# Kernel optimization log

Hardware: AMD Instinct MI355X
Metric: run time of the kernel (lower is better)

The kernel has to match this reference:

```python
import jax, jax.numpy as jnp
import numpy as np

N, E, G = 65536, 262144, 2048
DIN, H, F, L, P, TASK = 9, 300, 32, 5, 3, 1
DG = H + F + 1024 + 167  # 1523


def setup_inputs() -> dict:
    key = jax.random.key(0)
    ks = jax.random.split(key, 24)
    s = 0.02
    inp = {
        'x': jax.random.normal(ks[0], (N, DIN), jnp.float32),
        'morgan': jax.random.uniform(ks[1], (G, 1024), jnp.float32),
        'maccs': jax.random.uniform(ks[2], (G, 167), jnp.float32),
        'edge_index': jax.random.randint(ks[3], (2, E), 0, N, jnp.int32),
        'batch': jnp.sort(jax.random.randint(ks[4], (N,), 0, G, jnp.int32)),
        # node feature encoder
        'W_emb': s * jax.random.normal(ks[5], (DIN, H), jnp.float32),
        'b_emb': jnp.zeros((H,), jnp.float32),
        # GIN conv MLPs (L layers): H -> 2H -> H
        'gin_W1': s * jax.random.normal(ks[6], (L, H, 2 * H), jnp.float32),
        'gin_b1': jnp.zeros((L, 2 * H), jnp.float32),
        'gin_W2': s * jax.random.normal(ks[7], (L, 2 * H, H), jnp.float32),
        'gin_b2': jnp.zeros((L, H), jnp.float32),
        'bn_scale': jnp.ones((L, H), jnp.float32),
        'bn_bias': jnp.zeros((L, H), jnp.float32),
        'eps': jnp.zeros((L,), jnp.float32),
        # virtual node: init embedding + update MLPs (L-1 layers)
        'vn0': jnp.zeros((H,), jnp.float32),
        'vn_W1': s * jax.random.normal(ks[8], (L - 1, H, 2 * H), jnp.float32),
        'vn_b1': jnp.zeros((L - 1, 2 * H), jnp.float32),
        'vn_W2': s * jax.random.normal(ks[9], (L - 1, 2 * H, H), jnp.float32),
        'vn_b2': jnp.zeros((L - 1, H), jnp.float32),
        # predictor MLP: DG -> 2H -> TASK
        'Wp1': s * jax.random.normal(ks[10], (DG, 2 * H), jnp.float32),
        'bp1': jnp.zeros((2 * H,), jnp.float32),
        'Wp2': s * jax.random.normal(ks[11], (2 * H, TASK), jnp.float32),
        'bp2': jnp.zeros((TASK,), jnp.float32),
    }
    return inp


def _seg_mean(v, seg, n):
    s = jax.ops.segment_sum(v, seg, num_segments=n)
    c = jax.ops.segment_sum(jnp.ones((v.shape[0], 1), v.dtype), seg, num_segments=n)
    return s / jnp.maximum(c, 1.0)


def _bn(z, scale, bias):
    m = z.mean(0)
    v = z.var(0)
    return (z - m) * jax.lax.rsqrt(v + 1e-5) * scale + bias


def _gnn_and_predict(x, morgan, maccs, W_emb, b_emb, gin_W1, gin_b1, gin_W2, gin_b2,
                     bn_scale, bn_bias, eps, vn0, vn_W1, vn_b1, vn_W2, vn_b2,
                     Wp1, bp1, Wp2, bp2, edge_index, batch):
    n = x.shape[0]
    g = morgan.shape[0]
    nl = gin_W1.shape[0]
    src, dst = edge_index[0], edge_index[1]

    # GIN-virtual backbone (eval mode, dropout off). Note: GNN input is the
    # original x (the permuted ids are appended AFTER the GNN), so h is
    # permutation-independent and computed once.
    h = x @ W_emb + b_emb
    vn = jnp.broadcast_to(vn0, (g, vn0.shape[0]))
    for l in range(nl):
        hv = h + vn[batch]                                       # [N,H]
        agg = jax.ops.segment_sum(hv[src], dst, num_segments=n)  # neighbor sum
        z = (1.0 + eps[l]) * hv + agg
        z = jax.nn.relu(z @ gin_W1[l] + gin_b1[l]) @ gin_W2[l] + gin_b2[l]
        z = _bn(z, bn_scale[l], bn_bias[l])
        if l < nl - 1:
            z = jax.nn.relu(z)
        h = h + z  # residual
        if l < nl - 1:  # virtual node update
            vt = jax.ops.segment_sum(hv, batch, num_segments=g) + vn
            vn = vn + jax.nn.relu(jax.nn.relu(vt @ vn_W1[l] + vn_b1[l]) @ vn_W2[l] + vn_b2[l])

    pooled_h = _seg_mean(h, batch, g)  # [G,H]

    # Segmented random permutation of tiled eye(F) ids, averaged over P perms.
    # Each node gets one_hot(perm_rank_within_graph % F); rank computed by a
    # single lexsort over (batch, random) instead of a per-graph Python loop.
    counts = jax.ops.segment_sum(jnp.ones((n,), jnp.int32), batch, num_segments=g)
    starts = jnp.concatenate([jnp.zeros((1,), jnp.int32),
                              jnp.cumsum(counts)[:-1].astype(jnp.int32)])
    pkey = jax.random.key(42)
    acc = jnp.zeros((g, F), h.dtype)
    for p in range(P):
        r = jax.random.uniform(jax.random.fold_in(pkey, p), (n,))
        order = jnp.lexsort((r, batch))                       # sort by graph, then random
        local = jnp.arange(n, dtype=jnp.int32) - starts[batch[order]]
        rank = jnp.zeros((n,), jnp.int32).at[order].set(local)  # random rank in graph
        ids = jax.nn.one_hot(rank % F, F, dtype=h.dtype)        # [N,F]
        acc = acc + _seg_mean(ids, batch, g)
    id_pool = acc / P

    # h_rep order matches torch: [pooled h | pooled ids | morgan | maccs]
    h_rep = jnp.concatenate([pooled_h, id_pool, morgan, maccs], axis=1)  # [G,1523]
    return jax.nn.relu(h_rep @ Wp1 + bp1) @ Wp2 + bp2  # [G,TASK]


def reference(x, morgan, maccs, W_emb, b_emb, gin_W1, gin_b1, gin_W2, gin_b2,
              bn_scale, bn_bias, eps, vn0, vn_W1, vn_b1, vn_W2, vn_b2,
              Wp1, bp1, Wp2, bp2, edge_index, batch):
    return _gnn_and_predict(x, morgan, maccs, W_emb, b_emb, gin_W1, gin_b1,
                            gin_W2, gin_b2, bn_scale, bn_bias, eps, vn0,
                            vn_W1, vn_b1, vn_W2, vn_b2, Wp1, bp1, Wp2, bp2,
                            edge_index, batch)
```

## Files before the change

kernel.cpp:

```cpp
#include <hip/hip_runtime.h>

typedef unsigned short u16;
typedef unsigned int u32;
typedef __attribute__((ext_vector_type(8))) short bf16x8_t;
typedef __attribute__((ext_vector_type(4))) float f32x4_t;

#define kN 65536
#define kE 262144
#define kG 2048
#define kH 300
#define kH2 600
#define kL 5
#define kF 32
#define kDG 1523
#define KP_H 320
#define KP_H2 640
#define KP_DG 1536
#define NP_H2 640
#define NP_H 320
#define HVS 320
#define HVS32 160

__device__ __forceinline__ float bf2f(u16 x) {
    union { u32 u; float f; } v; v.u = ((u32)x) << 16; return v.f;
}
__device__ __forceinline__ u16 f2bf(float f) {
    union { float f; u32 u; } v; v.f = f;
    u32 u = v.u;
    u32 r = (u + 0x7fffu + ((u >> 16) & 1u)) >> 16;
    return (u16)r;
}
__device__ __forceinline__ float blo(u32 v) { return bf2f((u16)(v & 0xffffu)); }
__device__ __forceinline__ float bhi(u32 v) { return bf2f((u16)(v >> 16)); }
__device__ __forceinline__ u32 pack2(float lo, float hi) {
    return (u32)f2bf(lo) | ((u32)f2bf(hi) << 16);
}

__device__ __forceinline__ void gld16(const u16* g, u16* l) {
    __builtin_amdgcn_global_load_lds(
        (const __attribute__((address_space(1))) u32*)g,
        (__attribute__((address_space(3))) u32*)l, 16, 0, 0);
}

__device__ __forceinline__ void vwait4() { asm volatile("s_waitcnt vmcnt(4)" ::: "memory"); }
__device__ __forceinline__ void vwait6() { asm volatile("s_waitcnt vmcnt(6)" ::: "memory"); }
__device__ __forceinline__ void vwait8() { asm volatile("s_waitcnt vmcnt(8)" ::: "memory"); }
__device__ __forceinline__ void vwait0() { asm volatile("s_waitcnt vmcnt(0)" ::: "memory"); }
__device__ __forceinline__ void rbar() {
    __builtin_amdgcn_sched_barrier(0);
    __builtin_amdgcn_s_barrier();
    __builtin_amdgcn_sched_barrier(0);
}

__device__ __forceinline__ void swz_tile(int& m, int& n) {
    int p = blockIdx.x + gridDim.x * blockIdx.y;
    int xcd = p & 7;
    int q = p >> 3;
    int NB = gridDim.y;
    int mb8 = gridDim.x >> 3;
    m = xcd * mb8 + q / NB;
    n = q % NB;
}

__global__ void transpose_k(const float* __restrict__ W, u16* __restrict__ Wt,
                            int K, int NN, int NP, int KP, long total) {
    long idx = (long)blockIdx.x * 256 + threadIdx.x;
    if (idx >= total) return;
    int per = NP * KP;
    int b = (int)(idx / per);
    int r = (int)(idx % per);
    int n = r / KP;
    int k = r % KP;
    u16 v = 0;
    if (n < NN && k < K) v = f2bf(W[(long)b * K * NN + (long)k * NN + n]);
    Wt[idx] = v;
}

__global__ void hist_g_k(const int* __restrict__ batch, int* __restrict__ counts) {
    int n = blockIdx.x * 256 + threadIdx.x;
    if (n < kN) atomicAdd(&counts[batch[n]], 1);
}

__global__ void scan_g_k(const int* __restrict__ counts, int* __restrict__ starts) {
    __shared__ int s[1024];
    int t = threadIdx.x;
    int c0 = counts[2 * t], c1 = counts[2 * t + 1];
    s[t] = c0 + c1;
    __syncthreads();
    for (int off = 1; off < 1024; off <<= 1) {
        int v = (t >= off) ? s[t - off] : 0;
        __syncthreads();
        s[t] += v;
        __syncthreads();
    }
    int excl = (t > 0) ? s[t - 1] : 0;
    starts[2 * t] = excl;
    starts[2 * t + 1] = excl + c0;
}

__global__ void hist_n_k(const int* __restrict__ ei, int* __restrict__ cnt) {
    int e = blockIdx.x * 256 + threadIdx.x;
    if (e < kE) atomicAdd(&cnt[ei[kE + e]], 1);
}

__global__ void scanA_k(const int* __restrict__ cnt, int* __restrict__ start, int* __restrict__ bsum) {
    __shared__ int s[1024];
    int b = blockIdx.x, t = threadIdx.x;
    int v = cnt[b * 1024 + t];
    s[t] = v;
    __syncthreads();
    for (int off = 1; off < 1024; off <<= 1) {
        int u = (t >= off) ? s[t - off] : 0;
        __syncthreads();
        s[t] += u;
        __syncthreads();
    }
    start[b * 1024 + t] = s[t] - v;
    if (t == 1023) bsum[b] = s[1023];
}

__global__ void scanB_k(int* __restrict__ bsum) {
    if (threadIdx.x == 0) {
        int s = 0;
        for (int i = 0; i < kN / 1024; i++) { s += bsum[i]; bsum[i] = s; }
    }
}

__global__ void scanC_k(int* __restrict__ start, const int* __restrict__ bsum) {
    int b = blockIdx.x, t = threadIdx.x;
    int add = (b > 0) ? bsum[b - 1] : 0;
    start[b * 1024 + t] += add;
    if (b == kN / 1024 - 1 && t == 1023) start[kN] = bsum[kN / 1024 - 1];
}

__global__ void fill_n_k(const int* __restrict__ ei, const int* __restrict__ start,
                         int* __restrict__ fill, int* __restrict__ perm) {
    int e = blockIdx.x * 256 + threadIdx.x;
    if (e >= kE) return;
    int s = ei[e], d = ei[kE + e];
    int pos = start[d] + atomicAdd(&fill[d], 1);
    perm[pos] = s;
}

__global__ __launch_bounds__(256) void embed_k(
    const float* __restrict__ x, const float* __restrict__ W,
    const float* __restrict__ b, const float* __restrict__ vn0,
    u32* __restrict__ hv32) {
    __shared__ float sW[9 * kH];
    __shared__ float sBV[kH];
    int tid = threadIdx.x;
    for (int i = tid; i < 9 * kH; i += 256) sW[i] = W[i];
    for (int i = tid; i < kH; i += 256) sBV[i] = b[i] + vn0[i];
    __syncthreads();
    int wave = tid >> 6, lane = tid & 63;
    int n = blockIdx.x * 4 + wave;
    float xv[9];
    #pragma unroll
    for (int d = 0; d < 9; d++) xv[d] = x[n * 9 + d];
    #pragma unroll
    for (int p = 0; p < 3; p++) {
        int ii = lane + p * 64;
        if (ii < 150) {
            int c0 = 2 * ii;
            float a0 = sBV[c0], a1 = sBV[c0 + 1];
            #pragma unroll
            for (int d = 0; d < 9; d++) {
                a0 += xv[d] * sW[d * kH + c0];
                a1 += xv[d] * sW[d * kH + c0 + 1];
            }
            hv32[(long)n * HVS32 + ii] = pack2(a0, a1);
        } else if (ii < HVS32) {
            hv32[(long)n * HVS32 + ii] = 0u;
        }
    }
}

__global__ void vninit_k(const float* __restrict__ vn0, float* __restrict__ vn) {
    int g = blockIdx.x, c = threadIdx.x;
    if (c < kH) vn[g * kH + c] = vn0[c];
}

__global__ __launch_bounds__(256) void gather_combine_k(
    const u32* __restrict__ hv32, const int* __restrict__ start_n,
    const int* __restrict__ perm, const float* __restrict__ eps, int l,
    u32* __restrict__ out32, float* __restrict__ stats) {
    int tid = threadIdx.x;
    int wave = tid >> 6, lane = tid & 63;
    int n = blockIdx.x * 4 + wave;
    int st = start_n[n], en = start_n[n + 1];
    int i0 = lane, i1 = lane + 64, i2 = lane + 128;
    bool p2 = (i2 < 150);
    float a0 = 0.f, b0 = 0.f, a1 = 0.f, b1 = 0.f, a2 = 0.f, b2 = 0.f;
    int e = st;
    for (; e + 4 <= en; e += 4) {
        const u32* rA = hv32 + (long)perm[e] * HVS32;
        const u32* rB = hv32 + (long)perm[e + 1] * HVS32;
        const u32* rC = hv32 + (long)perm[e + 2] * HVS32;
        const u32* rD = hv32 + (long)perm[e + 3] * HVS32;
        u32 vA0 = rA[i0], vA1 = rA[i1], vA2 = p2 ? rA[i2] : 0u;
        u32 vB0 = rB[i0], vB1 = rB[i1], vB2 = p2 ? rB[i2] : 0u;
        u32 vC0 = rC[i0], vC1 = rC[i1], vC2 = p2 ? rC[i2] : 0u;
        u32 vD0 = rD[i0], vD1 = rD[i1], vD2 = p2 ? rD[i2] : 0u;
        a0 += (blo(vA0) + blo(vB0)) + (blo(vC0) + blo(vD0));
        b0 += (bhi(vA0) + bhi(vB0)) + (bhi(vC0) + bhi(vD0));
        a1 += (blo(vA1) + blo(vB1)) + (blo(vC1) + blo(vD1));
        b1 += (bhi(vA1) + bhi(vB1)) + (bhi(vC1) + bhi(vD1));
        a2 += (blo(vA2) + blo(vB2)) + (blo(vC2) + blo(vD2));
        b2 += (bhi(vA2) + bhi(vB2)) + (bhi(vC2) + bhi(vD2));
    }
    for (; e + 2 <= en; e += 2) {
        const u32* rA = hv32 + (long)perm[e] * HVS32;
        const u32* rB = hv32 + (long)perm[e + 1] * HVS32;
        u32 vA0 = rA[i0], vA1 = rA[i1], vA2 = p2 ? rA[i2] : 0u;
        u32 vB0 = rB[i0], vB1 = rB[i1], vB2 = p2 ? rB[i2] : 0u;
        a0 += blo(vA0) + blo(vB0); b0 += bhi(vA0) + bhi(vB0);
        a1 += blo(vA1) + blo(vB1); b1 += bhi(vA1) + bhi(vB1);
        a2 += blo(vA2) + blo(vB2); b2 += bhi(vA2) + bhi(vB2);
    }
    if (e < en) {
        const u32* rA = hv32 + (long)perm[e] * HVS32;
        u32 vA0 = rA[i0], vA1 = rA[i1], vA2 = p2 ? rA[i2] : 0u;
        a0 += blo(vA0); b0 += bhi(vA0);
        a1 += blo(vA1); b1 += bhi(vA1);
        a2 += blo(vA2); b2 += bhi(vA2);
    }
    const u32* self = hv32 + (long)n * HVS32;
    float ep = 1.f + eps[l];
    u32 s0 = self[i0], s1 = self[i1];
    u32* o = out32 + (long)n * HVS32;
    o[i0] = pack2(ep * blo(s0) + a0, ep * bhi(s0) + b0);
    o[i1] = pack2(ep * blo(s1) + a1, ep * bhi(s1) + b1);
    if (p2) {
        u32 s2 = self[i2];
        o[i2] = pack2(ep * blo(s2) + a2, ep * bhi(s2) + b2);
    } else if (i2 < HVS32) {
        o[i2] = 0u;
    }
    int gz = blockIdx.x * 256 + tid;
    if (gz < 2 * kH) stats[gz] = 0.f;
}

__global__ __launch_bounds__(256) void vt_fin_k(
    const u32* __restrict__ hv32, const float* __restrict__ vncur,
    const int* __restrict__ counts, const int* __restrict__ starts,
    u32* __restrict__ vt32) {
    int tid = threadIdx.x, wave = tid >> 6, lane = tid & 63;
    int g = blockIdx.x * 4 + wave;
    int cnt = counts[g], st = starts[g];
    int i0 = lane, i1 = lane + 64, i2 = lane + 128;
    bool p2 = (i2 < 150);
    float a0 = 0.f, b0 = 0.f, a1 = 0.f, b1 = 0.f, a2 = 0.f, b2 = 0.f;
    int i = 0;
    for (; i + 4 <= cnt; i += 4) {
        const u32* rA = hv32 + (long)(st + i) * HVS32;
        const u32* rB = hv32 + (long)(st + i + 1) * HVS32;
        const u32* rC = hv32 + (long)(st + i + 2) * HVS32;
        const u32* rD = hv32 + (long)(st + i + 3) * HVS32;
        u32 vA0 = rA[i0], vA1 = rA[i1], vA2 = p2 ? rA[i2] : 0u;
        u32 vB0 = rB[i0], vB1 = rB[i1], vB2 = p2 ? rB[i2] : 0u;
        u32 vC0 = rC[i0], vC1 = rC[i1], vC2 = p2 ? rC[i2] : 0u;
        u32 vD0 = rD[i0], vD1 = rD[i1], vD2 = p2 ? rD[i2] : 0u;
        a0 += (blo(vA0) + blo(vB0)) + (blo(vC0) + blo(vD0));
        b0 += (bhi(vA0) + bhi(vB0)) + (bhi(vC0) + bhi(vD0));
        a1 += (blo(vA1) + blo(vB1)) + (blo(vC1) + blo(vD1));
        b1 += (bhi(vA1) + bhi(vB1)) + (bhi(vC1) + bhi(vD1));
        a2 += (blo(vA2) + blo(vB2)) + (blo(vC2) + blo(vD2));
        b2 += (bhi(vA2) + bhi(vB2)) + (bhi(vC2) + bhi(vD2));
    }
    for (; i < cnt; i++) {
        const u32* rA = hv32 + (long)(st + i) * HVS32;
        u32 vA0 = rA[i0], vA1 = rA[i1], vA2 = p2 ? rA[i2] : 0u;
        a0 += blo(vA0); b0 += bhi(vA0);
        a1 += blo(vA1); b1 += bhi(vA1);
        a2 += blo(vA2); b2 += bhi(vA2);
    }
    const float* vg = vncur + g * kH;
    vt32[(long)g * HVS32 + i0] = pack2(a0 + vg[2 * i0], b0 + vg[2 * i0 + 1]);
    vt32[(long)g * HVS32 + i1] = pack2(a1 + vg[2 * i1], b1 + vg[2 * i1 + 1]);
    if (p2) vt32[(long)g * HVS32 + i2] = pack2(a2 + vg[2 * i2], b2 + vg[2 * i2 + 1]);
    else if (i2 < HVS32) vt32[(long)g * HVS32 + i2] = 0u;
}

__global__ __launch_bounds__(512, 2) void fused_mlp_k(
    const u16* __restrict__ A,
    const u16* __restrict__ W1t,
    const float* __restrict__ b1,
    const u16* __restrict__ W2t,
    const float* __restrict__ b2,
    u16* __restrict__ outp,
    float* __restrict__ stats) {
    __shared__ __align__(16) u16 lA[2][128 * 64];
    __shared__ __align__(16) u16 lW1[2][128 * 64];
    __shared__ __align__(16) u16 z1c[128 * 128];
    __shared__ __align__(16) u16 lW2[320 * 64];
    __shared__ float sred[320][2];

    const int tid = threadIdx.x;
    const int lane = tid & 63;
    const int wave = tid >> 6;
    const int l16 = lane & 15;
    const int quad = lane >> 4;
    const long tm = (long)blockIdx.x * 128;
    const int srow = lane >> 3;
    const int sch = (lane & 7) ^ srow;

    const int wm = (wave & 1) * 64;
    const int wnA = (wave >> 1) * 32;
    const int wnB = (wave >> 1) * 80;

    if (tid < 320) { sred[tid][0] = 0.f; sred[tid][1] = 0.f; }

    float rb1[5][2];
    #pragma unroll
    for (int c = 0; c < 5; c++)
        #pragma unroll
        for (int nt = 0; nt < 2; nt++) {
            int gc = c * 128 + wnA + nt * 16 + l16;
            rb1[c][nt] = (gc < kH2) ? b1[gc] : 0.f;
        }
    float rb2[5];
    #pragma unroll
    for (int nt = 0; nt < 5; nt++) {
        int col = wnB + nt * 16 + l16;
        rb2[nt] = (col < kH) ? b2[col] : 0.f;
    }

    f32x4_t acc2[4][5];
    #pragma unroll
    for (int i = 0; i < 4; i++)
        #pragma unroll
        for (int j = 0; j < 5; j++) acc2[i][j] = (f32x4_t){0.f, 0.f, 0.f, 0.f};

    for (int c = 0; c < 5; c++) {
        f32x4_t acc1[4][2];
        #pragma unroll
        for (int i = 0; i < 4; i++) {
            acc1[i][0] = (f32x4_t){0.f, 0.f, 0.f, 0.f};
            acc1[i][1] = (f32x4_t){0.f, 0.f, 0.f, 0.f};
        }
        auto stageA = [&](int bb, int k0) {
            #pragma unroll
            for (int j = 0; j < 2; j++) {
                int rb = wave * 16 + j * 8;
                gld16(A + (tm + rb + srow) * KP_H + k0 + sch * 8, &lA[bb][rb * 64]);
                gld16(W1t + (long)(c * 128 + rb + srow) * KP_H + k0 + sch * 8, &lW1[bb][rb * 64]);
            }
        };
        stageA(0, 0);
        stageA(1, 64);
        for (int t = 0; t < 5; t++) {
            if (t < 4) vwait4(); else vwait0();
            rbar();
            const u16* la = lA[t & 1];
            const u16* lw = lW1[t & 1];
            #pragma unroll
            for (int ks = 0; ks < 2; ks++) {
                bf16x8_t af[4], bfr[2];
                #pragma unroll
                for (int mt = 0; mt < 4; mt++) {
                    int row = wm + mt * 16 + l16;
                    int phys = (ks * 4 + quad) ^ (l16 & 7);
                    af[mt] = *(const bf16x8_t*)&la[row * 64 + phys * 8];
                }
                #pragma unroll
                for (int nt = 0; nt < 2; nt++) {
                    int row = wnA + nt * 16 + l16;
                    int phys = (ks * 4 + quad) ^ (l16 & 7);
                    bfr[nt] = *(const bf16x8_t*)&lw[row * 64 + phys * 8];
                }
                #pragma unroll
                for (int mt = 0; mt < 4; mt++)
                    #pragma unroll
                    for (int nt = 0; nt < 2; nt++)
                        acc1[mt][nt] = __builtin_amdgcn_mfma_f32_16x16x32_bf16(af[mt], bfr[nt], acc1[mt][nt], 0, 0, 0);
            }
            rbar();
            if (t + 2 < 5) stageA(t & 1, (t + 2) * 64);
        }

        #pragma unroll
        for (int j = 0; j < 5; j++) {
            int rb = wave * 40 + j * 8;
            gld16(W2t + (long)(rb + srow) * KP_H2 + c * 128 + sch * 8, &lW2[rb * 64]);
        }

        #pragma unroll
        for (int nt = 0; nt < 2; nt++) {
            int col = wnA + nt * 16 + l16;
            #pragma unroll
            for (int mt = 0; mt < 4; mt++) {
                #pragma unroll
                for (int r = 0; r < 4; r++) {
                    int row = wm + mt * 16 + quad * 4 + r;
                    float v = acc1[mt][nt][r] + rb1[c][nt];
                    v = fmaxf(v, 0.f);
                    int phys = (col >> 3) ^ (row & 15);
                    z1c[row * 128 + phys * 8 + (col & 7)] = f2bf(v);
                }
            }
        }
        __syncthreads();

        #pragma unroll
        for (int s = 0; s < 2; s++) {
            #pragma unroll
            for (int ks = 0; ks < 2; ks++) {
                bf16x8_t af[4], bfr[5];
                #pragma unroll
                for (int mt = 0; mt < 4; mt++) {
                    int row = wm + mt * 16 + l16;
                    int phys = (s * 8 + ks * 4 + quad) ^ (row & 15);
                    af[mt] = *(const bf16x8_t*)&z1c[row * 128 + phys * 8];
                }
                #pragma unroll
                for (int nt = 0; nt < 5; nt++) {
                    int row = wnB + nt * 16 + l16;
                    int phys = (ks * 4 + quad) ^ (l16 & 7);
                    bfr[nt] = *(const bf16x8_t*)&lW2[row * 64 + phys * 8];
                }
                #pragma unroll
                for (int mt = 0; mt < 4; mt++)
                    #pragma unroll
                    for (int nt = 0; nt < 5; nt++)
                        acc2[mt][nt] = __builtin_amdgcn_mfma_f32_16x16x32_bf16(af[mt], bfr[nt], acc2[mt][nt], 0, 0, 0);
            }
            rbar();
            if (s == 0) {
                #pragma unroll
                for (int j = 0; j < 5; j++) {
                    int rb = wave * 40 + j * 8;
                    gld16(W2t + (long)(rb + srow) * KP_H2 + c * 128 + 64 + sch * 8, &lW2[rb * 64]);
                }
                vwait0();
                rbar();
            }
        }
    }

    #pragma unroll
    for (int nt = 0; nt < 5; nt++) {
        int col = wnB + nt * 16 + l16;
        float s = 0.f, s2 = 0.f;
        #pragma unroll
        for (int mt = 0; mt < 4; mt++) {
            #pragma unroll
            for (int r = 0; r < 4; r++) {
                long row = tm + wm + mt * 16 + quad * 4 + r;
                float v = acc2[mt][nt][r] + rb2[nt];
                float sv = (col < kH) ? v : 0.f;
                outp[row * KP_H + col] = f2bf(sv);
                s += sv; s2 += sv * sv;
            }
        }
        atomicAdd(&sred[col][0], s);
        atomicAdd(&sred[col][1], s2);
    }
    __syncthreads();
    if (tid < kH) {
        atomicAdd(&stats[tid], sred[tid][0]);
        atomicAdd(&stats[kH + tid], sred[tid][1]);
    }
}

template<int ACT, int OUT_BF16, int BN_STATS>
__global__ __launch_bounds__(256) void gemm_k(
    const u16* __restrict__ A, const u16* __restrict__ Wt,
    const float* __restrict__ bias, void* __restrict__ out,
    float* __restrict__ stats,
    int KP, int NN, int out_stride, int store_cols) {
    __shared__ __align__(16) u16 lA[2][128 * 64];
    __shared__ __align__(16) u16 lB[2][128 * 64];
    __shared__ float sred[128][2];

    const int tid = threadIdx.x;
    const int lane = tid & 63;
    const int wave = tid >> 6;
    const int l16 = lane & 15;
    const int quad = lane >> 4;
    const int wm = (wave & 1) * 64;
    const int wn = (wave >> 1) * 64;
    int sm, sn;
    swz_tile(sm, sn);
    const long tm = (long)sm * 128;
    const int tn = sn * 128;

    const int srow = lane >> 3;
    const int sch = (lane & 7) ^ srow;

    f32x4_t acc[4][4];
    #pragma unroll
    for (int i = 0; i < 4; i++)
        #pragma unroll
        for (int j = 0; j < 4; j++) acc[i][j] = (f32x4_t){0.f, 0.f, 0.f, 0.f};

    auto stage = [&](int bb, int k0) {
        #pragma unroll
        for (int j = 0; j < 4; j++) {
            int rb = wave * 32 + j * 8;
            int r = rb + srow;
            gld16(A + (tm + r) * KP + k0 + sch * 8, &lA[bb][rb * 64]);
            gld16(Wt + (long)(tn + r) * KP + k0 + sch * 8, &lB[bb][rb * 64]);
        }
    };

    const int nk = KP >> 6;
    stage(0, 0);
    if (nk > 1) stage(1, 64);
    for (int t = 0; t < nk; t++) {
        if (t < nk - 1) vwait8(); else vwait0();
        rbar();
        const u16* la = lA[t & 1];
        const u16* lb = lB[t & 1];
        #pragma unroll
        for (int ks = 0; ks < 2; ks++) {
            bf16x8_t af[4], bfr[4];
            #pragma unroll
            for (int mt = 0; mt < 4; mt++) {
                int row = wm + mt * 16 + l16;
                int phys = (ks * 4 + quad) ^ (l16 & 7);
                af[mt] = *(const bf16x8_t*)&la[row * 64 + phys * 8];
            }
            #pragma unroll
            for (int nt = 0; nt < 4; nt++) {
                int row = wn + nt * 16 + l16;
                int phys = (ks * 4 + quad) ^ (l16 & 7);
                bfr[nt] = *(const bf16x8_t*)&lb[row * 64 + phys * 8];
            }
            #pragma unroll
            for (int mt = 0; mt < 4; mt++)
                #pragma unroll
                for (int nt = 0; nt < 4; nt++)
                    acc[mt][nt] = __builtin_amdgcn_mfma_f32_16x16x32_bf16(af[mt], bfr[nt], acc[mt][nt], 0, 0, 0);
        }
        rbar();
        if (t + 2 < nk) stage(t & 1, (t + 2) * 64);
    }

    if (BN_STATS) {
        if (tid < 128) { sred[tid][0] = 0.f; sred[tid][1] = 0.f; }
    }
    __syncthreads();

    #pragma unroll
    for (int nt = 0; nt < 4; nt++) {
        int col = tn + wn + nt * 16 + l16;
        float bv = (col < NN) ? bias[col] : 0.f;
        float s = 0.f, s2 = 0.f;
        #pragma unroll
        for (int mt = 0; mt < 4; mt++) {
            #pragma unroll
            for (int r = 0; r < 4; r++) {
                long row = tm + wm + mt * 16 + quad * 4 + r;
                float v = acc[mt][nt][r] + bv;
                if (ACT) v = fmaxf(v, 0.f);
                float sv = (col < NN) ? v : 0.f;
                if (col < store_cols) {
                    if (OUT_BF16) ((u16*)out)[row * out_stride + col] = f2bf(sv);
                    else          ((float*)out)[row * out_stride + col] = sv;
                }
                s += sv; s2 += sv * sv;
            }
        }
        if (BN_STATS) {
            atomicAdd(&sred[wn + nt * 16 + l16][0], s);
            atomicAdd(&sred[wn + nt * 16 + l16][1], s2);
        }
    }
    if (BN_STATS) {
        __syncthreads();
        if (tid < 128) {
            int col = tn + tid;
            if (col < NN) {
                atomicAdd(&stats[col], sred[tid][0]);
                atomicAdd(&stats[NN + col], sred[tid][1]);
            }
        }
    }
}

template<int ACT, int OUT_MODE, int BN_STATS>
__global__ __launch_bounds__(256) void gemm64_k(
    const u16* __restrict__ A, const u16* __restrict__ Wt,
    const float* __restrict__ bias, void* __restrict__ out,
    float* __restrict__ stats, const float* __restrict__ vnacc,
    int KP, int NN, int out_stride, int store_cols) {
    __shared__ __align__(16) u16 lA[2][128 * 64];
    __shared__ __align__(16) u16 lB[2][64 * 64];
    __shared__ float sred[64][2];

    const int tid = threadIdx.x;
    const int lane = tid & 63;
    const int wave = tid >> 6;
    const int l16 = lane & 15;
    const int quad = lane >> 4;
    const int wm = (wave & 1) * 64;
    const int wn = (wave >> 1) * 32;
    int sm, sn;
    swz_tile(sm, sn);
    const long tm = (long)sm * 128;
    const int tn = sn * 64;

    const int srow = lane >> 3;
    const int sch = (lane & 7) ^ srow;

    f32x4_t acc[4][2];
    #pragma unroll
    for (int i = 0; i < 4; i++)
        #pragma unroll
        for (int j = 0; j < 2; j++) acc[i][j] = (f32x4_t){0.f, 0.f, 0.f, 0.f};

    auto stage = [&](int bb, int k0) {
        #pragma unroll
        for (int j = 0; j < 4; j++) {
            int rb = wave * 32 + j * 8;
            gld16(A + (tm + rb + srow) * KP + k0 + sch * 8, &lA[bb][rb * 64]);
        }
        #pragma unroll
        for (int j = 0; j < 2; j++) {
            int rb = wave * 16 + j * 8;
            gld16(Wt + (long)(tn + rb + srow) * KP + k0 + sch * 8, &lB[bb][rb * 64]);
        }
    };

    const int nk = KP >> 6;
    stage(0, 0);
    if (nk > 1) stage(1, 64);
    for (int t = 0; t < nk; t++) {
        if (t < nk - 1) vwait6(); else vwait0();
        rbar();
        const u16* la = lA[t & 1];
        const u16* lb = lB[t & 1];
        #pragma unroll
        for (int ks = 0; ks < 2; ks++) {
            bf16x8_t af[4], bfr[2];
            #pragma unroll
            for (int mt = 0; mt < 4; mt++) {
                int row = wm + mt * 16 + l16;
                int phys = (ks * 4 + quad) ^ (l16 & 7);
                af[mt] = *(const bf16x8_t*)&la[row * 64 + phys * 8];
            }
            #pragma unroll
            for (int nt = 0; nt < 2; nt++) {
                int row = wn + nt * 16 + l16;
                int phys = (ks * 4 + quad) ^ (l16 & 7);
                bfr[nt] = *(const bf16x8_t*)&lb[row * 64 + phys * 8];
            }
            #pragma unroll
            for (int mt = 0; mt < 4; mt++)
                #pragma unroll
                for (int nt = 0; nt < 2; nt++)
                    acc[mt][nt] = __builtin_amdgcn_mfma_f32_16x16x32_bf16(af[mt], bfr[nt], acc[mt][nt], 0, 0, 0);
        }
        rbar();
        if (t + 2 < nk) stage(t & 1, (t + 2) * 64);
    }

    if (BN_STATS) {
        if (tid < 64) { sred[tid][0] = 0.f; sred[tid][1] = 0.f; }
    }
    __syncthreads();

    #pragma unroll
    for (int nt = 0; nt < 2; nt++) {
        int col = tn + wn + nt * 16 + l16;
        float bv = (col < NN) ? bias[col] : 0.f;
        float s = 0.f, s2 = 0.f;
        #pragma unroll
        for (int mt = 0; mt < 4; mt++) {
            #pragma unroll
            for (int r = 0; r < 4; r++) {
                long row = tm + wm + mt * 16 + quad * 4 + r;
                float v = acc[mt][nt][r] + bv;
                if (ACT) v = fmaxf(v, 0.f);
                float sv = (col < NN) ? v : 0.f;
                if (col < store_cols) {
                    if (OUT_MODE == 1) ((u16*)out)[row * out_stride + col] = f2bf(sv);
                    else if (OUT_MODE == 2)
                        ((float*)out)[row * out_stride + col] =
                            vnacc[row * out_stride + col] + fmaxf(v, 0.f);
                    else ((float*)out)[row * out_stride + col] = sv;
                }
                s += sv; s2 += sv * sv;
            }
        }
        if (BN_STATS) {
            atomicAdd(&sred[wn + nt * 16 + l16][0], s);
            atomicAdd(&sred[wn + nt * 16 + l16][1], s2);
        }
    }
    if (BN_STATS) {
        __syncthreads();
        if (tid < 64) {
            int col = tn + tid;
            if (col < NN) {
                atomicAdd(&stats[col], sred[tid][0]);
                atomicAdd(&stats[NN + col], sred[tid][1]);
            }
        }
    }
}

template<int RELU>
__global__ __launch_bounds__(256) void resid_k(
    u32* __restrict__ hvb32, const u32* __restrict__ z32,
    const float* __restrict__ stats,
    const float* __restrict__ scale, const float* __restrict__ bias, int l,
    const int* __restrict__ batch,
    const float* __restrict__ vncur, const float* __restrict__ vnnxt) {
    int tid = threadIdx.x;
    int wave = tid >> 6, lane = tid & 63;
    int n = blockIdx.x * 4 + wave;
    int g = batch[n];
    #pragma unroll
    for (int p = 0; p < 3; p++) {
        int ii = lane + p * 64;
        if (ii >= 150) break;
        int c0 = 2 * ii;
        float m0 = stats[c0] * (1.f / (float)kN), m1 = stats[c0 + 1] * (1.f / (float)kN);
        float v0 = fmaxf(stats[kH + c0] * (1.f / (float)kN) - m0 * m0, 0.f);
        float v1 = fmaxf(stats[kH + c0 + 1] * (1.f / (float)kN) - m1 * m1, 0.f);
        float a0 = scale[l * kH + c0] * rsqrtf(v0 + 1e-5f);
        float a1 = scale[l * kH + c0 + 1] * rsqrtf(v1 + 1e-5f);
        float d0 = bias[l * kH + c0] - m0 * a0;
        float d1 = bias[l * kH + c0 + 1] - m1 * a1;
        u32 zz = z32[(long)n * HVS32 + ii];
        u32 ho = hvb32[(long)n * HVS32 + ii];
        float2 vc = *(const float2*)(vncur + g * kH + c0);
        float2 vx = *(const float2*)(vnnxt + g * kH + c0);
        float t0 = blo(zz) * a0 + d0;
        float t1 = bhi(zz) * a1 + d1;
        if (RELU) { t0 = fmaxf(t0, 0.f); t1 = fmaxf(t1, 0.f); }
        float h0 = (blo(ho) - vc.x) + t0;
        float h1 = (bhi(ho) - vc.y) + t1;
        hvb32[(long)n * HVS32 + ii] = pack2(h0 + vx.x, h1 + vx.y);
    }
}

__global__ __launch_bounds__(256) void pooled_k(
    const u32* __restrict__ hv32, const float* __restrict__ vnlast,
    const int* __restrict__ counts, const int* __restrict__ starts,
    u32* __restrict__ hrep32) {
    int tid = threadIdx.x, wave = tid >> 6, lane = tid & 63;
    int g = blockIdx.x * 4 + wave;
    int cnt = counts[g], st = starts[g];
    int i0 = lane, i1 = lane + 64, i2 = lane + 128;
    bool p2 = (i2 < 150);
    float a0 = 0.f, b0 = 0.f, a1 = 0.f, b1 = 0.f, a2 = 0.f, b2 = 0.f;
    int i = 0;
    for (; i + 4 <= cnt; i += 4) {
        const u32* rA = hv32 + (long)(st + i) * HVS32;
        const u32* rB = hv32 + (long)(st + i + 1) * HVS32;
        const u32* rC = hv32 + (long)(st + i + 2) * HVS32;
        const u32* rD = hv32 + (long)(st + i + 3) * HVS32;
        u32 vA0 = rA[i0], vA1 = rA[i1], vA2 = p2 ? rA[i2] : 0u;
        u32 vB0 = rB[i0], vB1 = rB[i1], vB2 = p2 ? rB[i2] : 0u;
        u32 vC0 = rC[i0], vC1 = rC[i1], vC2 = p2 ? rC[i2] : 0u;
        u32 vD0 = rD[i0], vD1 = rD[i1], vD2 = p2 ? rD[i2] : 0u;
        a0 += (blo(vA0) + blo(vB0)) + (blo(vC0) + blo(vD0));
        b0 += (bhi(vA0) + bhi(vB0)) + (bhi(vC0) + bhi(vD0));
        a1 += (blo(vA1) + blo(vB1)) + (blo(vC1) + blo(vD1));
        b1 += (bhi(vA1) + bhi(vB1)) + (bhi(vC1) + bhi(vD1));
        a2 += (blo(vA2) + blo(vB2)) + (blo(vC2) + blo(vD2));
        b2 += (bhi(vA2) + bhi(vB2)) + (bhi(vC2) + bhi(vD2));
    }
    for (; i < cnt; i++) {
        const u32* rA = hv32 + (long)(st + i) * HVS32;
        u32 vA0 = rA[i0], vA1 = rA[i1], vA2 = p2 ? rA[i2] : 0u;
        a0 += blo(vA0); b0 += bhi(vA0);
        a1 += blo(vA1); b1 += bhi(vA1);
        a2 += blo(vA2); b2 += bhi(vA2);
    }
    float fc = (float)cnt;
    float inv = 1.f / (float)(cnt > 0 ? cnt : 1);
    const float* vg = vnlast + g * kH;
    hrep32[(long)g * 768 + i0] = pack2((a0 - fc * vg[2 * i0]) * inv, (b0 - fc * vg[2 * i0 + 1]) * inv);
    hrep32[(long)g * 768 + i1] = pack2((a1 - fc * vg[2 * i1]) * inv, (b1 - fc * vg[2 * i1 + 1]) * inv);
    if (p2)
        hrep32[(long)g * 768 + i2] = pack2((a2 - fc * vg[2 * i2]) * inv, (b2 - fc * vg[2 * i2 + 1]) * inv);
}

__global__ void hrep_rest_k(const float* __restrict__ morgan, const float* __restrict__ maccs,
                            const int* __restrict__ counts, u16* __restrict__ hrep) {
    long idx = (long)blockIdx.x * 256 + threadIdx.x;
    if (idx >= (long)kG * (KP_DG - kH)) return;
    int g = (int)(idx / (KP_DG - kH));
    int j = (int)(idx % (KP_DG - kH));
    int col = kH + j;
    u16 v;
    if (j < kF) {
        int c = counts[g];
        int q = (j < c) ? ((c - 1 - j) / kF + 1) : 0;
        v = f2bf((float)q / (float)(c > 0 ? c : 1));
    } else if (j < kF + 1024) {
        v = f2bf(morgan[(long)g * 1024 + (j - kF)]);
    } else if (j < kF + 1024 + 167) {
        v = f2bf(maccs[(long)g * 167 + (j - kF - 1024)]);
    } else {
        v = 0;
    }
    hrep[(long)g * KP_DG + col] = v;
}

__global__ void final_k(const u16* __restrict__ zp, const float* __restrict__ Wp2,
                        const float* __restrict__ bp2, float* __restrict__ out) {
    int wave = threadIdx.x >> 6, lane = threadIdx.x & 63;
    int g = blockIdx.x * 4 + wave;
    float acc = 0.f;
    for (int c = lane; c < kH2; c += 64) acc += bf2f(zp[(long)g * KP_H2 + c]) * Wp2[c];
    #pragma unroll
    for (int off = 32; off; off >>= 1) acc += __shfl_down(acc, off);
    if (lane == 0) out[g] = acc + bp2[0];
}

extern "C" void kernel_launch(void* const* d_in, const int* in_sizes, int n_in,
                              void* d_out, int out_size, void* d_ws, size_t ws_size,
                              hipStream_t stream) {
    const float* x      = (const float*)d_in[0];
    const float* morgan = (const float*)d_in[1];
    const float* maccs  = (const float*)d_in[2];
    const int*   ei     = (const int*)d_in[3];
    const int*   batch  = (const int*)d_in[4];
    const float* W_emb  = (const float*)d_in[5];
    const float* b_emb  = (const float*)d_in[6];
    const float* gin_W1 = (const float*)d_in[7];
    const float* gin_b1 = (const float*)d_in[8];
    const float* gin_W2 = (const float*)d_in[9];
    const float* gin_b2 = (const float*)d_in[10];
    const float* bn_scale = (const float*)d_in[11];
    const float* bn_bias  = (const float*)d_in[12];
    const float* eps    = (const float*)d_in[13];
    const float* vn0    = (const float*)d_in[14];
    const float* vn_W1  = (const float*)d_in[15];
    const float* vn_b1  = (const float*)d_in[16];
    const float* vn_W2  = (const float*)d_in[17];
    const float* vn_b2  = (const float*)d_in[18];
    const float* Wp1    = (const float*)d_in[19];
    const float* bp1    = (const float*)d_in[20];
    const float* Wp2    = (const float*)d_in[21];
    const float* bp2    = (const float*)d_in[22];
    float* out = (float*)d_out;

    char* ws = (char*)d_ws;
    size_t off = 0;
    auto alloc = [&](size_t bytes) -> char* {
        char* p = ws + off;
        off += (bytes + 255) & ~(size_t)255;
        return p;
    };
    u16*   hvbf = (u16*)alloc((size_t)kN * HVS * 2);
    u16*   hv   = (u16*)alloc((size_t)kN * KP_H * 2);
    u16*   z1   = (u16*)alloc((size_t)kN * KP_H2 * 2);
    float* vnA  = (float*)alloc((size_t)kG * kH * 4);
    float* vnB  = (float*)alloc((size_t)kG * kH * 4);
    int* counts = (int*)alloc(kG * 4);
    int* starts = (int*)alloc(kG * 4);
    float* stats = (float*)alloc(2 * kH * 4);
    int* cnt_n  = (int*)alloc((size_t)kN * 4);
    int* start_n = (int*)alloc((size_t)(kN + 1) * 4);
    int* fill_n = (int*)alloc((size_t)kN * 4);
    int* bsum   = (int*)alloc((kN / 1024) * 4);
    int* perm   = (int*)alloc((size_t)kE * 4);
    u16* Wt_g1 = (u16*)alloc((size_t)kL * NP_H2 * KP_H * 2);
    u16* Wt_g2 = (u16*)alloc((size_t)kL * NP_H * KP_H2 * 2);
    u16* Wt_v1 = (u16*)alloc((size_t)(kL - 1) * NP_H2 * KP_H * 2);
    u16* Wt_v2 = (u16*)alloc((size_t)(kL - 1) * NP_H * KP_H2 * 2);
    u16* Wt_p1 = (u16*)alloc((size_t)NP_H2 * KP_DG * 2);
    if (off > ws_size) return;

    u16* vt_in = z1;
    u16* z1v   = z1 + (size_t)4 * 1024 * 1024;
    u16* hrep  = z1;
    u16* zp    = z1 + (size_t)8 * 1024 * 1024;
    float* vnb[2] = {vnA, vnB};

    {
        long t1 = (long)kL * NP_H2 * KP_H;
        transpose_k<<<dim3((unsigned)((t1 + 255) / 256)), 256, 0, stream>>>(gin_W1, Wt_g1, kH, kH2, NP_H2, KP_H, t1);
        long t2 = (long)kL * NP_H * KP_H2;
        transpose_k<<<dim3((unsigned)((t2 + 255) / 256)), 256, 0, stream>>>(gin_W2, Wt_g2, kH2, kH, NP_H, KP_H2, t2);
        long t3 = (long)(kL - 1) * NP_H2 * KP_H;
        transpose_k<<<dim3((unsigned)((t3 + 255) / 256)), 256, 0, stream>>>(vn_W1, Wt_v1, kH, kH2, NP_H2, KP_H, t3);
        long t4 = (long)(kL - 1) * NP_H * KP_H2;
        transpose_k<<<dim3((unsigned)((t4 + 255) / 256)), 256, 0, stream>>>(vn_W2, Wt_v2, kH2, kH, NP_H, KP_H2, t4);
        long t5 = (long)NP_H2 * KP_DG;
        transpose_k<<<dim3((unsigned)((t5 + 255) / 256)), 256, 0, stream>>>(Wp1, Wt_p1, kDG, kH2, NP_H2, KP_DG, t5);
    }

    hipMemsetAsync(counts, 0, kG * 4, stream);
    hipMemsetAsync(cnt_n, 0, (size_t)kN * 4, stream);
    hipMemsetAsync(fill_n, 0, (size_t)kN * 4, stream);
    hist_g_k<<<kN / 256, 256, 0, stream>>>(batch, counts);
    scan_g_k<<<1, 1024, 0, stream>>>(counts, starts);
    hist_n_k<<<kE / 256, 256, 0, stream>>>(ei, cnt_n);
    scanA_k<<<kN / 1024, 1024, 0, stream>>>(cnt_n, start_n, bsum);
    scanB_k<<<1, 64, 0, stream>>>(bsum);
    scanC_k<<<kN / 1024, 1024, 0, stream>>>(start_n, bsum);
    fill_n_k<<<kE / 256, 256, 0, stream>>>(ei, start_n, fill_n, perm);

    embed_k<<<kN / 4, 256, 0, stream>>>(x, W_emb, b_emb, vn0, (u32*)hvbf);
    vninit_k<<<kG, 320, 0, stream>>>(vn0, vnA);

    for (int l = 0; l < kL; l++) {
        float* vcur = vnb[l & 1];
        float* vnxt = vnb[(l + 1) & 1];
        gather_combine_k<<<kN / 4, 256, 0, stream>>>(
            (const u32*)hvbf, start_n, perm, eps, l, (u32*)hv, stats);
        if (l < kL - 1) {
            vt_fin_k<<<kG / 4, 256, 0, stream>>>(
                (const u32*)hvbf, vcur, counts, starts, (u32*)vt_in);
            gemm_k<1, 1, 0><<<dim3(16, NP_H2 / 128), 256, 0, stream>>>(
                vt_in, Wt_v1 + (size_t)l * NP_H2 * KP_H, vn_b1 + l * kH2,
                z1v, nullptr, KP_H, kH2, KP_H2, KP_H2);
            gemm64_k<0, 2, 0><<<dim3(16, NP_H / 64), 256, 0, stream>>>(
                z1v, Wt_v2 + (size_t)l * NP_H * KP_H2, vn_b2 + l * kH,
                vnxt, nullptr, vcur, KP_H2, kH, kH, kH);
        }
        fused_mlp_k<<<kN / 128, 512, 0, stream>>>(
            hv, Wt_g1 + (size_t)l * NP_H2 * KP_H, gin_b1 + l * kH2,
            Wt_g2 + (size_t)l * NP_H * KP_H2, gin_b2 + l * kH,
            hv, stats);
        if (l < kL - 1)
            resid_k<1><<<kN / 4, 256, 0, stream>>>(
                (u32*)hvbf, (const u32*)hv, stats, bn_scale, bn_bias, l, batch, vcur, vnxt);
        else
            resid_k<0><<<kN / 4, 256, 0, stream>>>(
                (u32*)hvbf, (const u32*)hv, stats, bn_scale, bn_bias, l, batch, vcur, vcur);
    }

    float* vnlast = vnb[(kL - 1) & 1];
    pooled_k<<<kG / 4, 256, 0, stream>>>(
        (const u32*)hvbf, vnlast, counts, starts, (u32*)hrep);
    {
        long tr = (long)kG * (KP_DG - kH);
        hrep_rest_k<<<dim3((unsigned)((tr + 255) / 256)), 256, 0, stream>>>(morgan, maccs, counts, hrep);
    }
    gemm_k<1, 1, 0><<<dim3(16, NP_H2 / 128), 256, 0, stream>>>(
        hrep, Wt_p1, bp1, zp, nullptr, KP_DG, kH2, KP_H2, KP_H2);
    final_k<<<kG / 4, 256, 0, stream>>>(zp, Wp2, bp2, out);
}
```

Baseline: 1.309 ms.

## Keep full A tile resident in LDS and load weights directly into registers

```diff
diff --git a/kernel.cpp b/kernel.cpp
--- a/kernel.cpp
+++ b/kernel.cpp
@@ -42,10 +42,10 @@
         (__attribute__((address_space(3))) u32*)l, 16, 0, 0);
 }
 
-__device__ __forceinline__ void vwait4() { asm volatile("s_waitcnt vmcnt(4)" ::: "memory"); }
 __device__ __forceinline__ void vwait6() { asm volatile("s_waitcnt vmcnt(6)" ::: "memory"); }
 __device__ __forceinline__ void vwait8() { asm volatile("s_waitcnt vmcnt(8)" ::: "memory"); }
 __device__ __forceinline__ void vwait0() { asm volatile("s_waitcnt vmcnt(0)" ::: "memory"); }
+__device__ __forceinline__ void lwait0() { asm volatile("s_waitcnt lgkmcnt(0)" ::: "memory"); }
 __device__ __forceinline__ void rbar() {
     __builtin_amdgcn_sched_barrier(0);
     __builtin_amdgcn_s_barrier();
@@ -289,10 +289,8 @@
     const float* __restrict__ b2,
     u16* __restrict__ outp,
     float* __restrict__ stats) {
-    __shared__ __align__(16) u16 lA[2][128 * 64];
-    __shared__ __align__(16) u16 lW1[2][128 * 64];
+    __shared__ __align__(16) u16 lA[5][128 * 64];
     __shared__ __align__(16) u16 z1c[128 * 128];
-    __shared__ __align__(16) u16 lW2[320 * 64];
     __shared__ float sred[320][2];
 
     const int tid = threadIdx.x;
@@ -310,6 +308,15 @@
 
     if (tid < 320) { sred[tid][0] = 0.f; sred[tid][1] = 0.f; }
 
+    #pragma unroll
+    for (int t = 0; t < 5; t++) {
+        #pragma unroll
+        for (int j = 0; j < 2; j++) {
+            int rb = wave * 16 + j * 8;
+            gld16(A + (tm + rb + srow) * KP_H + t * 64 + sch * 8, &lA[t][rb * 64]);
+        }
+    }
+
     float rb1[5][2];
     #pragma unroll
     for (int c = 0; c < 5; c++)
@@ -331,6 +338,9 @@
         #pragma unroll
         for (int j = 0; j < 5; j++) acc2[i][j] = (f32x4_t){0.f, 0.f, 0.f, 0.f};
 
+    vwait0();
+    rbar();
+
     for (int c = 0; c < 5; c++) {
         f32x4_t acc1[4][2];
         #pragma unroll
@@ -338,52 +348,38 @@
             acc1[i][0] = (f32x4_t){0.f, 0.f, 0.f, 0.f};
             acc1[i][1] = (f32x4_t){0.f, 0.f, 0.f, 0.f};
         }
-        auto stageA = [&](int bb, int k0) {
-            #pragma unroll
-            for (int j = 0; j < 2; j++) {
-                int rb = wave * 16 + j * 8;
-                gld16(A + (tm + rb + srow) * KP_H + k0 + sch * 8, &lA[bb][rb * 64]);
-                gld16(W1t + (long)(c * 128 + rb + srow) * KP_H + k0 + sch * 8, &lW1[bb][rb * 64]);
-            }
-        };
-        stageA(0, 0);
-        stageA(1, 64);
-        for (int t = 0; t < 5; t++) {
-            if (t < 4) vwait4(); else vwait0();
-            rbar();
-            const u16* la = lA[t & 1];
-            const u16* lw = lW1[t & 1];
-            #pragma unroll
-            for (int ks = 0; ks < 2; ks++) {
-                bf16x8_t af[4], bfr[2];
-                #pragma unroll
-                for (int mt = 0; mt < 4; mt++) {
-                    int row = wm + mt * 16 + l16;
-                    int phys = (ks * 4 + quad) ^ (l16 & 7);
-                    af[mt] = *(const bf16x8_t*)&la[row * 64 + phys * 8];
-                }
-                #pragma unroll
-                for (int nt = 0; nt < 2; nt++) {
-                    int row = wnA + nt * 16 + l16;
-                    int phys = (ks * 4 + quad) ^ (l16 & 7);
-                    bfr[nt] = *(const bf16x8_t*)&lw[row * 64 + phys * 8];
-                }
-                #pragma unroll
-                for (int mt = 0; mt < 4; mt++)
-                    #pragma unroll
-                    for (int nt = 0; nt < 2; nt++)
-                        acc1[mt][nt] = __builtin_amdgcn_mfma_f32_16x16x32_bf16(af[mt], bfr[nt], acc1[mt][nt], 0, 0, 0);
-            }
-            rbar();
-            if (t + 2 < 5) stageA(t & 1, (t + 2) * 64);
-        }
-
-        #pragma unroll
-        for (int j = 0; j < 5; j++) {
-            int rb = wave * 40 + j * 8;
-            gld16(W2t + (long)(rb + srow) * KP_H2 + c * 128 + sch * 8, &lW2[rb * 64]);
-        }
-
+        const u16* w1p0 = W1t + (long)(c * 128 + wnA + l16) * KP_H + quad * 8;
+        const u16* w1p1 = w1p0 + 16 * KP_H;
+        bf16x8_t wf[3][2];
+        #pragma unroll
+        for (int p = 0; p < 2; p++) {
+            int kk = (p >> 1) * 64 + (p & 1) * 32;
+            wf[p][0] = *(const bf16x8_t*)(w1p0 + kk);
+            wf[p][1] = *(const bf16x8_t*)(w1p1 + kk);
+        }
+        #pragma unroll
+        for (int tk = 0; tk < 10; tk++) {
+            if (tk + 2 < 10) {
+                int kk = ((tk + 2) >> 1) * 64 + ((tk + 2) & 1) * 32;
+                wf[(tk + 2) % 3][0] = *(const bf16x8_t*)(w1p0 + kk);
+                wf[(tk + 2) % 3][1] = *(const bf16x8_t*)(w1p1 + kk);
+            }
+            const int t = tk >> 1, ks = tk & 1;
+            bf16x8_t af[4];
+            #pragma unroll
+            for (int mt = 0; mt < 4; mt++) {
+                int row = wm + mt * 16 + l16;
+                int phys = (ks * 4 + quad) ^ (l16 & 7);
+                af[mt] = *(const bf16x8_t*)&lA[t][row * 64 + phys * 8];
+            }
+            #pragma unroll
+            for (int mt = 0; mt < 4; mt++) {
+                acc1[mt][0] = __builtin_amdgcn_mfma_f32_16x16x32_bf16(af[mt], wf[tk % 3][0], acc1[mt][0], 0, 0, 0);
+                acc1[mt][1] = __builtin_amdgcn_mfma_f32_16x16x32_bf16(af[mt], wf[tk % 3][1], acc1[mt][1], 0, 0, 0);
+            }
+        }
+
+        rbar();
         #pragma unroll
         for (int nt = 0; nt < 2; nt++) {
             int col = wnA + nt * 16 + l16;
@@ -392,48 +388,39 @@
                 #pragma unroll
                 for (int r = 0; r < 4; r++) {
                     int row = wm + mt * 16 + quad * 4 + r;
-                    float v = acc1[mt][nt][r] + rb1[c][nt];
-                    v = fmaxf(v, 0.f);
+                    float v = fmaxf(acc1[mt][nt][r] + rb1[c][nt], 0.f);
                     int phys = (col >> 3) ^ (row & 15);
                     z1c[row * 128 + phys * 8 + (col & 7)] = f2bf(v);
                 }
             }
         }
-        __syncthreads();
-
-        #pragma unroll
-        for (int s = 0; s < 2; s++) {
-            #pragma unroll
-            for (int ks = 0; ks < 2; ks++) {
-                bf16x8_t af[4], bfr[5];
+        lwait0();
+        rbar();
+
+        const u16* w2p = W2t + (long)(wnB + l16) * KP_H2 + c * 128 + quad * 8;
+        bf16x8_t wg[2][5];
+        #pragma unroll
+        for (int nt = 0; nt < 5; nt++)
+            wg[0][nt] = *(const bf16x8_t*)(w2p + (long)nt * 16 * KP_H2);
+        #pragma unroll
+        for (int ks = 0; ks < 4; ks++) {
+            if (ks + 1 < 4) {
                 #pragma unroll
-                for (int mt = 0; mt < 4; mt++) {
-                    int row = wm + mt * 16 + l16;
-                    int phys = (s * 8 + ks * 4 + quad) ^ (row & 15);
-                    af[mt] = *(const bf16x8_t*)&z1c[row * 128 + phys * 8];
-                }
+                for (int nt = 0; nt < 5; nt++)
+                    wg[(ks + 1) & 1][nt] = *(const bf16x8_t*)(w2p + (long)nt * 16 * KP_H2 + (ks + 1) * 32);
+            }
+            bf16x8_t af[4];
+            #pragma unroll
+            for (int mt = 0; mt < 4; mt++) {
+                int row = wm + mt * 16 + l16;
+                int phys = (ks * 4 + quad) ^ (row & 15);
+                af[mt] = *(const bf16x8_t*)&z1c[row * 128 + phys * 8];
+            }
+            #pragma unroll
+            for (int mt = 0; mt < 4; mt++)
                 #pragma unroll
-                for (int nt = 0; nt < 5; nt++) {
-                    int row = wnB + nt * 16 + l16;
-                    int phys = (ks * 4 + quad) ^ (l16 & 7);
-                    bfr[nt] = *(const bf16x8_t*)&lW2[row * 64 + phys * 8];
-                }
-                #pragma unroll
-                for (int mt = 0; mt < 4; mt++)
-                    #pragma unroll
-                    for (int nt = 0; nt < 5; nt++)
-                        acc2[mt][nt] = __builtin_amdgcn_mfma_f32_16x16x32_bf16(af[mt], bfr[nt], acc2[mt][nt], 0, 0, 0);
-            }
-            rbar();
-            if (s == 0) {
-                #pragma unroll
-                for (int j = 0; j < 5; j++) {
-                    int rb = wave * 40 + j * 8;
-                    gld16(W2t + (long)(rb + srow) * KP_H2 + c * 128 + 64 + sch * 8, &lW2[rb * 64]);
-                }
-                vwait0();
-                rbar();
-            }
+                for (int nt = 0; nt < 5; nt++)
+                    acc2[mt][nt] = __builtin_amdgcn_mfma_f32_16x16x32_bf16(af[mt], wg[ks & 1][nt], acc2[mt][nt], 0, 0, 0);
         }
     }
 
```

Result: slower. 1.454 ms (+11.1%).
